# Kernel optimization log

Measured on AMD Instinct MI355X. Metric: run time of the kernel, lower is better.

The kernel has to match this reference:

```python
import jax, jax.numpy as jnp
import numpy as np

N_EMBD = 768
NUM_HEADS = 12
HEAD_DIM = 64
B, S = 4, 2048


def setup_inputs() -> dict:
    key = jax.random.key(0)
    ks = jax.random.split(key, 9)
    scale = 1.0 / np.sqrt(N_EMBD)
    def lin(k):
        kw, kb = jax.random.split(k)
        W = jax.random.uniform(kw, (N_EMBD, N_EMBD), jnp.float32, -scale, scale)
        b = jax.random.uniform(kb, (N_EMBD,), jnp.float32, -scale, scale)
        return W, b
    wq_w, wq_b = lin(ks[0])
    wk_w, wk_b = lin(ks[1])
    wv_w, wv_b = lin(ks[2])
    wo_w, wo_b = lin(ks[3])
    x = jax.random.normal(ks[4], (B, S, N_EMBD), jnp.float32)
    return {
        "x": x,
        "wq_w": wq_w, "wq_b": wq_b,
        "wk_w": wk_w, "wk_b": wk_b,
        "wv_w": wv_w, "wv_b": wv_b,
        "wo_w": wo_w, "wo_b": wo_b,
    }


def reference(x, wq_w, wq_b, wk_w, wk_b, wv_w, wv_b, wo_w, wo_b):
    bs, sl, dim = x.shape
    # Linear projections (torch Linear: x @ W.T + b)
    q = x @ wq_w.T + wq_b
    k = x @ wk_w.T + wk_b
    v = x @ wv_w.T + wv_b
    # [B, S, H, D] -> [B, H, S, D]
    q = q.reshape(bs, sl, NUM_HEADS, HEAD_DIM).transpose(0, 2, 1, 3)
    k = k.reshape(bs, sl, NUM_HEADS, HEAD_DIM).transpose(0, 2, 1, 3)
    v = v.reshape(bs, sl, NUM_HEADS, HEAD_DIM).transpose(0, 2, 1, 3)
    # scores: [B, H, S, S]
    attn = jnp.einsum("bhqd,bhkd->bhqk", q, k) / jnp.sqrt(jnp.float32(HEAD_DIM))
    attn = jax.nn.softmax(attn, axis=-1)
    # dropout is identity in eval mode (reference baseline)
    out = jnp.einsum("bhqk,bhkd->bhqd", attn, v)  # [B, H, S, D]
    out = out.transpose(0, 2, 1, 3).reshape(bs, sl, dim)
    return out @ wo_w.T + wo_b
```

## Files before the change

kernel.cpp:

```cpp
#include <hip/hip_runtime.h>
#include <stdint.h>
#include <stddef.h>

#define NEMBD 768
#define NH    12
#define HD    64
#define SEQ   2048
#define TOK   8192
#define QKVN  2304
#define NT    (SEQ / 64)
#define QSCALE 0.18033688011112042f

typedef __attribute__((ext_vector_type(4))) float f32x4;
typedef __attribute__((ext_vector_type(8))) __bf16 bf8;
typedef __attribute__((ext_vector_type(8))) short s16x8;
typedef __attribute__((ext_vector_type(4))) short s16x4;

static __device__ __forceinline__ short f2bf(float f) {
  __bf16 h = (__bf16)f;
  union { __bf16 h; short s; } u; u.h = h; return u.s;
}

typedef const __attribute__((address_space(1))) unsigned int* gp1;
typedef __attribute__((address_space(3))) unsigned int* lp3;
static __device__ __forceinline__ void gload_lds16(const void* g, void* l) {
  __builtin_amdgcn_global_load_lds((gp1)g, (lp3)l, 16, 0, 0);
}

__global__ __launch_bounds__(256) void prep_kern(
    const float* __restrict__ x, short* __restrict__ xb,
    const float* __restrict__ wq, const float* __restrict__ wk, const float* __restrict__ wv,
    const float* __restrict__ wo, const float* __restrict__ bq, const float* __restrict__ bk,
    const float* __restrict__ bv, short* __restrict__ wqkv, short* __restrict__ wo16,
    float* __restrict__ bqkv) {
  const int WN = NEMBD * NEMBD;
  int blk = blockIdx.x;
  if (blk < 6144) {
    int i = (blk * 256 + threadIdx.x) * 4;
    f32x4 v = *(const f32x4*)(x + i);
    s16x4 o;
#pragma unroll
    for (int j = 0; j < 4; ++j) o[j] = f2bf(v[j]);
    *(s16x4*)(xb + i) = o;
    return;
  }
  int t = (blk - 6144) * 256 + threadIdx.x;
  const int n4 = WN;
  if (t < n4) {
    int i4 = t * 4;
    const float* src; short* dst; int rem;
    if (i4 < 3 * WN) {
      int which = i4 / WN;
      rem = i4 - which * WN;
      src = which == 0 ? wq : (which == 1 ? wk : wv);
      dst = wqkv + i4;
    } else {
      rem = i4 - 3 * WN;
      src = wo;
      dst = wo16 + rem;
    }
    f32x4 v = *(const f32x4*)(src + rem);
    s16x4 o;
#pragma unroll
    for (int j = 0; j < 4; ++j) o[j] = f2bf(v[j]);
    *(s16x4*)dst = o;
  } else {
    int t2 = t - n4;
    if (t2 < QKVN) {
      int which = t2 / NEMBD, rem = t2 - which * NEMBD;
      bqkv[t2] = (which == 0 ? bq : (which == 1 ? bk : bv))[rem];
    }
  }
}

template <int EPI, int BN>
__global__ __launch_bounds__(256) void gemm128(
    const short* __restrict__ A, const short* __restrict__ Bw, const float* __restrict__ bias,
    short* __restrict__ q_out, short* __restrict__ k_out, short* __restrict__ v_out,
    float* __restrict__ c_out, int M, int N, int K) {
  __shared__ short As[128 * 64];
  __shared__ short Bs[BN * 64];
  const int NFR = BN / 32;
  const int tid = threadIdx.x;
  const int wave = tid >> 6, lane = tid & 63;
  const int r = lane & 15, g = lane >> 4;

  const int nwg = gridDim.x * gridDim.y;
  const int bid = blockIdx.y * gridDim.x + blockIdx.x;
  const int sb = (bid & 7) * (nwg >> 3) + (bid >> 3);
  const int bx = sb % gridDim.x, by = sb / gridDim.x;

  const int n0 = bx * BN, m0 = by * 128;
  const int wm0 = (wave >> 1) * 64, wn0 = (wave & 1) * (BN / 2);
  const int lrow = lane >> 3;
  const int lcol = ((lane & 7) ^ (lane >> 3)) * 8;
  const int cbr = (r & 7) << 4;

  f32x4 acc[4][NFR];
#pragma unroll
  for (int mi = 0; mi < 4; ++mi)
#pragma unroll
    for (int ni = 0; ni < NFR; ++ni) acc[mi][ni] = (f32x4){0.f, 0.f, 0.f, 0.f};

  for (int kt = 0; kt < K; kt += 64) {
#pragma unroll
    for (int ii = 0; ii < 4; ++ii) {
      int blk = wave * 4 + ii;
      gload_lds16(A + (size_t)(m0 + blk * 8 + lrow) * K + kt + lcol, &As[blk * 512]);
    }
#pragma unroll
    for (int ii = 0; ii < BN / 32; ++ii) {
      int blk = wave * (BN / 32) + ii;
      gload_lds16(Bw + (size_t)(n0 + blk * 8 + lrow) * K + kt + lcol, &Bs[blk * 512]);
    }
    __syncthreads();
#pragma unroll
    for (int kk = 0; kk < 2; ++kk) {
      int cb = (kk * 64 + g * 16) ^ cbr;
      bf8 af[4], bfv[NFR];
#pragma unroll
      for (int mi = 0; mi < 4; ++mi)
        af[mi] = *(const bf8*)((const char*)As + (wm0 + 16 * mi + r) * 128 + cb);
#pragma unroll
      for (int ni = 0; ni < NFR; ++ni)
        bfv[ni] = *(const bf8*)((const char*)Bs + (wn0 + 16 * ni + r) * 128 + cb);
#pragma unroll
      for (int mi = 0; mi < 4; ++mi)
#pragma unroll
        for (int ni = 0; ni < NFR; ++ni) {
          if (EPI == 1)
            acc[mi][ni] = __builtin_amdgcn_mfma_f32_16x16x32_bf16(af[mi], bfv[ni], acc[mi][ni], 0, 0, 0);
          else
            acc[mi][ni] = __builtin_amdgcn_mfma_f32_16x16x32_bf16(bfv[ni], af[mi], acc[mi][ni], 0, 0, 0);
        }
    }
    __syncthreads();
  }

  if (EPI == 2) {
#pragma unroll
    for (int ni = 0; ni < NFR; ++ni) {
      int colb = n0 + wn0 + 16 * ni + 4 * g;
      f32x4 bv4 = *(const f32x4*)&bias[colb];
#pragma unroll
      for (int mi = 0; mi < 4; ++mi) {
        int row = m0 + wm0 + 16 * mi + r;
        f32x4 ov;
#pragma unroll
        for (int j = 0; j < 4; ++j) ov[j] = acc[mi][ni][j] + bv4[j];
        *(f32x4*)&c_out[(size_t)row * N + colb] = ov;
      }
    }
  } else if (EPI == 0) {
#pragma unroll
    for (int ni = 0; ni < NFR; ++ni) {
      int colb = n0 + wn0 + 16 * ni + 4 * g;
      int which = colb / NEMBD;
      int rem = colb - which * NEMBD;
      int h = rem >> 6, d0 = rem & 63;
      short* dst = which == 0 ? q_out : k_out;
      float sc = which == 0 ? QSCALE : 1.0f;
      f32x4 bv4 = *(const f32x4*)&bias[colb];
#pragma unroll
      for (int mi = 0; mi < 4; ++mi) {
        int row = m0 + wm0 + 16 * mi + r;
        int b = row >> 11, s = row & 2047;
        s16x4 pk;
#pragma unroll
        for (int j = 0; j < 4; ++j) pk[j] = f2bf((acc[mi][ni][j] + bv4[j]) * sc);
        *(s16x4*)&dst[(((size_t)(b * NH + h)) * SEQ + s) * HD + d0] = pk;
      }
    }
  } else {
#pragma unroll
    for (int ni = 0; ni < NFR; ++ni) {
      int col = n0 + wn0 + 16 * ni + r;
      float bcol = bias[col];
      int h = col >> 6, d = col & 63;
#pragma unroll
      for (int mi = 0; mi < 4; ++mi) {
        int s0 = m0 + wm0 + 16 * mi + 4 * g;
        int b = s0 >> 11, s = s0 & 2047;
        s16x4 pk;
#pragma unroll
        for (int j = 0; j < 4; ++j) pk[j] = f2bf(acc[mi][ni][j] + bcol);
        *(s16x4*)&v_out[(((size_t)(b * NH + h)) * HD + d) * SEQ + s] = pk;
      }
    }
  }
}

__global__ __launch_bounds__(512) void attn_kern(
    const short* __restrict__ Qg, const short* __restrict__ Kg, const short* __restrict__ Vtg,
    short* __restrict__ Ao) {
  __shared__ short Kl[64 * 64];
  __shared__ short Vl[64 * 64];
  __shared__ short Pl[8][16 * 64];

  const int tid = threadIdx.x;
  const int wave = tid >> 6, lane = tid & 63;
  const int r = lane & 15, g = lane >> 4;

  const int nwg = gridDim.x * gridDim.y;
  const int bid = blockIdx.y * gridDim.x + blockIdx.x;
  const int sb = (bid & 7) * (nwg >> 3) + (bid >> 3);
  const int bh = sb >> 4;
  const int q0 = (sb & 15) * 128;
  const size_t base = (size_t)bh * (SEQ * HD);

  bf8 qf[2];
#pragma unroll
  for (int kk = 0; kk < 2; ++kk)
    qf[kk] = *(const bf8*)&Qg[base + (size_t)(q0 + wave * 16 + r) * HD + kk * 32 + g * 8];

  union { short s; __bf16 h; } one_u; one_u.s = 0x3F80;
  bf8 vones;
#pragma unroll
  for (int i = 0; i < 8; ++i) vones[i] = one_u.h;

  f32x4 o[4], osum;
#pragma unroll
  for (int fd = 0; fd < 4; ++fd) o[fd] = (f32x4){0.f, 0.f, 0.f, 0.f};
  osum = (f32x4){0.f, 0.f, 0.f, 0.f};

  const int cbr = (r & 7) << 4;
  short* Pw = &Pl[wave][0];

  const int srow = tid >> 3;
  const int sc8 = ((tid & 7) ^ (srow & 7)) * 8;

  for (int t = 0; t < NT; ++t) {
    gload_lds16(Kg + base + (size_t)(t * 64 + srow) * HD + sc8, &Kl[wave * 512]);
    gload_lds16(Vtg + base + (size_t)srow * SEQ + t * 64 + sc8, &Vl[wave * 512]);
    __syncthreads();

    f32x4 sv[4];
#pragma unroll
    for (int f = 0; f < 4; ++f) sv[f] = (f32x4){0.f, 0.f, 0.f, 0.f};
    __builtin_amdgcn_s_setprio(1);
#pragma unroll
    for (int kk = 0; kk < 2; ++kk) {
      int cb = (kk * 64 + g * 16) ^ cbr;
#pragma unroll
      for (int f = 0; f < 4; ++f) {
        bf8 kf = *(const bf8*)((const char*)Kl + (16 * f + r) * 128 + cb);
        sv[f] = __builtin_amdgcn_mfma_f32_16x16x32_bf16(kf, qf[kk], sv[f], 0, 0, 0);
      }
    }
    __builtin_amdgcn_s_setprio(0);

#pragma unroll
    for (int f = 0; f < 4; ++f) {
      s16x4 pk;
#pragma unroll
      for (int j = 0; j < 4; ++j)
        pk[j] = f2bf(__builtin_amdgcn_exp2f(sv[f][j]));
      *(s16x4*)((char*)Pw + r * 128 + ((32 * f + 8 * g) ^ cbr)) = pk;
    }

    __builtin_amdgcn_s_setprio(1);
#pragma unroll
    for (int kk = 0; kk < 2; ++kk) {
      bf8 pa = *(const bf8*)((const char*)Pw + r * 128 + ((64 * kk + 16 * g) ^ cbr));
      int cb = (kk * 64 + g * 16) ^ cbr;
      osum = __builtin_amdgcn_mfma_f32_16x16x32_bf16(pa, vones, osum, 0, 0, 0);
#pragma unroll
      for (int fd = 0; fd < 4; ++fd) {
        bf8 vb = *(const bf8*)((const char*)Vl + (16 * fd + r) * 128 + cb);
        o[fd] = __builtin_amdgcn_mfma_f32_16x16x32_bf16(pa, vb, o[fd], 0, 0, 0);
      }
    }
    __builtin_amdgcn_s_setprio(0);
    __syncthreads();
  }

  const int b = bh / NH, h = bh - b * NH;
#pragma unroll
  for (int j = 0; j < 4; ++j) {
    float ij = 1.f / osum[j];
    int srow_o = q0 + wave * 16 + 4 * g + j;
    size_t obase = ((size_t)(b * SEQ + srow_o)) * NEMBD + h * HD;
#pragma unroll
    for (int fd = 0; fd < 4; ++fd)
      Ao[obase + 16 * fd + r] = f2bf(o[fd][j] * ij);
  }
}

extern "C" void kernel_launch(void* const* d_in, const int* in_sizes, int n_in,
                              void* d_out, int out_size, void* d_ws, size_t ws_size,
                              hipStream_t stream) {
  (void)in_sizes; (void)n_in; (void)out_size; (void)ws_size;
  const float* x   = (const float*)d_in[0];
  const float* wqw = (const float*)d_in[1];
  const float* wqb = (const float*)d_in[2];
  const float* wkw = (const float*)d_in[3];
  const float* wkb = (const float*)d_in[4];
  const float* wvw = (const float*)d_in[5];
  const float* wvb = (const float*)d_in[6];
  const float* wow = (const float*)d_in[7];
  const float* wob = (const float*)d_in[8];

  char* ws = (char*)d_ws;
  short* xb   = (short*)(ws + 0);
  short* wqkv = (short*)(ws + 12582912);
  short* wo16 = (short*)(ws + 16121856);
  float* bqkv = (float*)(ws + 17301504);
  short* qb   = (short*)(ws + 17310720);
  short* kb   = (short*)(ws + 29893632);
  short* vb   = (short*)(ws + 42476544);

  prep_kern<<<dim3(6144 + 2313), dim3(256), 0, stream>>>(
      x, xb, wqw, wkw, wvw, wow, wqb, wkb, wvb, wqkv, wo16, bqkv);
  gemm128<0, 128><<<dim3(12, TOK / 128), dim3(256), 0, stream>>>(
      xb, wqkv, bqkv, qb, kb, nullptr, nullptr, TOK, QKVN, NEMBD);
  gemm128<1, 64><<<dim3(12, TOK / 128), dim3(256), 0, stream>>>(
      xb, wqkv + (size_t)2 * NEMBD * NEMBD, bqkv + 2 * NEMBD, nullptr, nullptr, vb,
      nullptr, TOK, QKVN, NEMBD);
  attn_kern<<<dim3(SEQ / 128, 48), dim3(512), 0, stream>>>(qb, kb, vb, xb);
  gemm128<2, 64><<<dim3(NEMBD / 64, TOK / 128), dim3(256), 0, stream>>>(
      xb, wo16, wob, nullptr, nullptr, nullptr, (float*)d_out, TOK, NEMBD, NEMBD);
}
```

Baseline: 145.9 us.

## Double-buffer K/V tiles in attention kernel to overlap loads with MFMA

Splits the K and V shared-memory tiles into two buffers and prefetches the next tile while computing on the current one. This replaces the old load, sync, compute, sync pattern with one barrier per tile, so global-to-LDS latency is meant to hide behind the QK and PV MFMA work. It doubles LDS use for K/V, which may lower occupancy. Correctness relies on the async LDS loads completing before the barrier that precedes each use.

```diff
diff --git a/kernel.cpp b/kernel.cpp
--- a/kernel.cpp
+++ b/kernel.cpp
@@ -193,8 +193,8 @@
 __global__ __launch_bounds__(512) void attn_kern(
     const short* __restrict__ Qg, const short* __restrict__ Kg, const short* __restrict__ Vtg,
     short* __restrict__ Ao) {
-  __shared__ short Kl[64 * 64];
-  __shared__ short Vl[64 * 64];
+  __shared__ short Kl[2][64 * 64];
+  __shared__ short Vl[2][64 * 64];
   __shared__ short Pl[8][16 * 64];
 
   const int tid = threadIdx.x;
@@ -229,49 +229,52 @@
   const int srow = tid >> 3;
   const int sc8 = ((tid & 7) ^ (srow & 7)) * 8;
 
-  for (int t = 0; t < NT; ++t) {
-    gload_lds16(Kg + base + (size_t)(t * 64 + srow) * HD + sc8, &Kl[wave * 512]);
-    gload_lds16(Vtg + base + (size_t)srow * SEQ + t * 64 + sc8, &Vl[wave * 512]);
+#define ASTAGE(T, KB, VB)                                                              \
+  {                                                                                    \
+    gload_lds16(Kg + base + (size_t)((T) * 64 + srow) * HD + sc8, (KB) + wave * 512);  \
+    gload_lds16(Vtg + base + (size_t)srow * SEQ + (T) * 64 + sc8, (VB) + wave * 512);  \
+  }
+
+#define ATILE(KB, VB)                                                                  \
+  {                                                                                    \
+    f32x4 sv[4];                                                                       \
+    _Pragma("unroll") for (int f = 0; f < 4; ++f) sv[f] = (f32x4){0.f, 0.f, 0.f, 0.f}; \
+    __builtin_amdgcn_s_setprio(1);                                                     \
+    _Pragma("unroll") for (int kk = 0; kk < 2; ++kk) {                                 \
+      int cb = (kk * 64 + g * 16) ^ cbr;                                               \
+      _Pragma("unroll") for (int f = 0; f < 4; ++f) {                                  \
+        bf8 kf = *(const bf8*)((const char*)(KB) + (16 * f + r) * 128 + cb);           \
+        sv[f] = __builtin_amdgcn_mfma_f32_16x16x32_bf16(kf, qf[kk], sv[f], 0, 0, 0);   \
+      }                                                                                \
+    }                                                                                  \
+    __builtin_amdgcn_s_setprio(0);                                                     \
+    _Pragma("unroll") for (int f = 0; f < 4; ++f) {                                    \
+      s16x4 pk;                                                                        \
+      _Pragma("unroll") for (int j = 0; j < 4; ++j)                                    \
+        pk[j] = f2bf(__builtin_amdgcn_exp2f(sv[f][j]));                                \
+      *(s16x4*)((char*)Pw + r * 128 + ((32 * f + 8 * g) ^ cbr)) = pk;                  \
+    }                                                                                  \
+    __builtin_amdgcn_s_setprio(1);                                                     \
+    _Pragma("unroll") for (int kk = 0; kk < 2; ++kk) {                                 \
+      bf8 pa = *(const bf8*)((const char*)Pw + r * 128 + ((64 * kk + 16 * g) ^ cbr));  \
+      int cb = (kk * 64 + g * 16) ^ cbr;                                               \
+      osum = __builtin_amdgcn_mfma_f32_16x16x32_bf16(pa, vones, osum, 0, 0, 0);        \
+      _Pragma("unroll") for (int fd = 0; fd < 4; ++fd) {                               \
+        bf8 vb = *(const bf8*)((const char*)(VB) + (16 * fd + r) * 128 + cb);          \
+        o[fd] = __builtin_amdgcn_mfma_f32_16x16x32_bf16(pa, vb, o[fd], 0, 0, 0);       \
+      }                                                                                \
+    }                                                                                  \
+    __builtin_amdgcn_s_setprio(0);                                                     \
+  }
+
+  ASTAGE(0, &Kl[0][0], &Vl[0][0]);
+  for (int t = 0; t < NT; t += 2) {
     __syncthreads();
-
-    f32x4 sv[4];
-#pragma unroll
-    for (int f = 0; f < 4; ++f) sv[f] = (f32x4){0.f, 0.f, 0.f, 0.f};
-    __builtin_amdgcn_s_setprio(1);
-#pragma unroll
-    for (int kk = 0; kk < 2; ++kk) {
-      int cb = (kk * 64 + g * 16) ^ cbr;
-#pragma unroll
-      for (int f = 0; f < 4; ++f) {
-        bf8 kf = *(const bf8*)((const char*)Kl + (16 * f + r) * 128 + cb);
-        sv[f] = __builtin_amdgcn_mfma_f32_16x16x32_bf16(kf, qf[kk], sv[f], 0, 0, 0);
-      }
-    }
-    __builtin_amdgcn_s_setprio(0);
-
-#pragma unroll
-    for (int f = 0; f < 4; ++f) {
-      s16x4 pk;
-#pragma unroll
-      for (int j = 0; j < 4; ++j)
-        pk[j] = f2bf(__builtin_amdgcn_exp2f(sv[f][j]));
-      *(s16x4*)((char*)Pw + r * 128 + ((32 * f + 8 * g) ^ cbr)) = pk;
-    }
-
-    __builtin_amdgcn_s_setprio(1);
-#pragma unroll
-    for (int kk = 0; kk < 2; ++kk) {
-      bf8 pa = *(const bf8*)((const char*)Pw + r * 128 + ((64 * kk + 16 * g) ^ cbr));
-      int cb = (kk * 64 + g * 16) ^ cbr;
-      osum = __builtin_amdgcn_mfma_f32_16x16x32_bf16(pa, vones, osum, 0, 0, 0);
-#pragma unroll
-      for (int fd = 0; fd < 4; ++fd) {
-        bf8 vb = *(const bf8*)((const char*)Vl + (16 * fd + r) * 128 + cb);
-        o[fd] = __builtin_amdgcn_mfma_f32_16x16x32_bf16(pa, vb, o[fd], 0, 0, 0);
-      }
-    }
-    __builtin_amdgcn_s_setprio(0);
+    if (t + 1 < NT) ASTAGE(t + 1, &Kl[1][0], &Vl[1][0]);
+    ATILE(&Kl[0][0], &Vl[0][0]);
     __syncthreads();
+    if (t + 2 < NT) ASTAGE(t + 2, &Kl[0][0], &Vl[0][0]);
+    ATILE(&Kl[1][0], &Vl[1][0]);
   }
 
   const int b = bh / NH, h = bh - b * NH;
```

Measured after the change: 156.7 us. +7.5%, slower.
